# Kernel tuning notes

Hardware: AMD Instinct MI355X
Metric: run time of the kernel (lower is better)

The kernel has to match this reference:

```python
import jax, jax.numpy as jnp
import numpy as np

B, T, I, H, O = 64, 2048, 128, 256, 128
K1 = 1
K2 = 1


def setup_inputs() -> dict:
    key = jax.random.key(0)
    ks = jax.random.split(key, 8)
    M = H - K1 + 1
    return {
        "x": jax.random.normal(ks[0], (B, T, I), jnp.float32),
        "W_in": jax.random.normal(ks[1], (H, I), jnp.float32) / np.sqrt(I).astype(np.float32),
        "b_in": jax.random.normal(ks[2], (H,), jnp.float32) * 0.01,
        "W_out": jax.random.normal(ks[3], (O, H), jnp.float32) / np.sqrt(H).astype(np.float32),
        "b_out": jax.random.normal(ks[4], (O,), jnp.float32) * 0.01,
        # padded Householder vectors: row i uses its first K+i entries (masked in reference)
        # uniform in [0.5, 1.5] keeps u.u well away from 0 (avoids 2/<u,u> blowup)
        "u_raw": jax.random.uniform(ks[5], (M, H), jnp.float32, 0.5, 1.5),
        "sigmas": jnp.ones((H,), jnp.float32),
        "v_raw": jax.random.uniform(ks[6], (M, H), jnp.float32, 0.5, 1.5),
    }


def _householder_chain(hats):
    # U <- H_last @ ... @ H_0, H_i = I - 2/<u,u> u u^T, applied as rank-1 updates
    Hdim = hats.shape[1]
    def step(Umat, u):
        beta = 2.0 / jnp.dot(u, u)
        return Umat - beta * jnp.outer(u, u @ Umat), None
    U, _ = jax.lax.scan(step, jnp.eye(Hdim, dtype=hats.dtype), hats)
    return U


def reference(x, W_in, b_in, W_out, b_out, u_raw, sigmas, v_raw):
    Hdim = sigmas.shape[0]
    Mu = u_raw.shape[0]
    Mv = v_raw.shape[0]
    # row i of u_hats has entries in cols [0, K1+i), then flipped along cols
    mask_u = jnp.arange(Hdim)[None, :] < (K1 + jnp.arange(Mu))[:, None]
    u_hats = jnp.flip(jnp.where(mask_u, u_raw, 0.0), axis=1)
    mask_v = jnp.arange(Hdim)[None, :] < (K2 + jnp.arange(Mv))[:, None]
    v_hats = jnp.flip(jnp.where(mask_v, v_raw, 0.0), axis=(0, 1))  # torch.flip dims=[0,1]
    U = _householder_chain(u_hats)
    V = _householder_chain(v_hats)
    W = (U * sigmas[None, :]) @ V  # U @ diag(sigmas) @ V
    # precompute input projection for all timesteps: [T, B, H]
    xproj = jnp.einsum('bti,hi->tbh', x, W_in) + b_in
    h0 = jnp.zeros((x.shape[0], Hdim), x.dtype)
    def cell(h, xp):
        h = jnp.tanh(xp + h @ W.T)
        return h, h @ W_out.T + b_out
    _, out = jax.lax.scan(cell, h0, xproj)  # out: [T, B, O]
    return jnp.transpose(out, (1, 0, 2))
```

## Files before the change

### kernel.cpp

```cpp
#include <hip/hip_runtime.h>
#include <hip/hip_bf16.h>
#include <hip/hip_fp16.h>

#define BB 64
#define TT 2048
#define II 128
#define HH 256
#define OO 128
#define RCH 8

typedef _Float16 f16x2 __attribute__((ext_vector_type(2)));

#if __has_builtin(__builtin_amdgcn_fdot2)
__device__ __forceinline__ float fdot2(f16x2 a, f16x2 b, float c) {
    return __builtin_amdgcn_fdot2(a, b, c, false);
}
#else
__device__ __forceinline__ float fdot2(f16x2 a, f16x2 b, float c) {
    return fmaf((float)a.x, (float)b.x, fmaf((float)a.y, (float)b.y, c));
}
#endif

__device__ __forceinline__ f16x2 u2h(unsigned int u) { return __builtin_bit_cast(f16x2, u); }
__device__ __forceinline__ unsigned int packf16(float a, float b) {
    return __builtin_bit_cast(unsigned int, f16x2{(_Float16)a, (_Float16)b});
}

__device__ __forceinline__ float tanh_fast(float x) {
    float xc = fminf(fmaxf(x, -9.0f), 9.0f);
    float e = __expf(2.0f * xc);
    return (e - 1.0f) * __fdividef(1.0f, e + 1.0f);
}

__global__ __launch_bounds__(64) void prep_kernel(
    const float* __restrict__ u_raw, const float* __restrict__ v_raw,
    float* __restrict__ u_eff, float* __restrict__ v_eff,
    float* __restrict__ beta_u, float* __restrict__ beta_v)
{
    const int row = blockIdx.x;
    const int lane = threadIdx.x;
    const bool isU = row < HH;
    const int i = isU ? row : row - HH;
    const float* src = isU ? (u_raw + (size_t)i * HH) : (v_raw + (size_t)(HH - 1 - i) * HH);
    float* dst = (isU ? u_eff : v_eff) + (size_t)i * HH;
    const int lo = isU ? (HH - 1 - i) : i;
    float ss = 0.0f;
    for (int c = lane; c < HH; c += 64) {
        float vv = (c >= lo) ? src[HH - 1 - c] : 0.0f;
        dst[c] = vv;
        ss += vv * vv;
    }
    for (int m = 1; m < 64; m <<= 1) ss += __shfl_xor(ss, m, 64);
    if (lane == 0) (isU ? beta_u : beta_v)[i] = 2.0f / ss;
}

__global__ __launch_bounds__(256) void hh_kernel(
    const float* __restrict__ u_eff, const float* __restrict__ v_eff,
    const float* __restrict__ beta_u, const float* __restrict__ beta_v,
    float* __restrict__ Ucol, float* __restrict__ Vrow)
{
    const int wid = blockIdx.x * 4 + (threadIdx.x >> 6);
    const int lane = threadIdx.x & 63;
    const bool isU = wid < HH;
    const int j = isU ? wid : wid - HH;
    const float* eff = isU ? u_eff : v_eff;
    const float* beta = isU ? beta_u : beta_v;

    float cr0 = (j == 4 * lane + 0) ? 1.0f : 0.0f;
    float cr1 = (j == 4 * lane + 1) ? 1.0f : 0.0f;
    float cr2 = (j == 4 * lane + 2) ? 1.0f : 0.0f;
    float cr3 = (j == 4 * lane + 3) ? 1.0f : 0.0f;

    const int i0 = isU ? (HH - 1 - j) : 0;
    for (int i = i0; i < HH; ++i) {
        const float4 v4 = *(const float4*)(eff + (size_t)i * HH + lane * 4);
        float d = v4.x * cr0 + v4.y * cr1 + v4.z * cr2 + v4.w * cr3;
        for (int m = 1; m < 64; m <<= 1) d += __shfl_xor(d, m, 64);
        const float t = beta[i] * d;
        cr0 = fmaf(-t, v4.x, cr0);
        cr1 = fmaf(-t, v4.y, cr1);
        cr2 = fmaf(-t, v4.z, cr2);
        cr3 = fmaf(-t, v4.w, cr3);
    }
    if (isU) {
        *(float4*)(Ucol + (size_t)j * HH + lane * 4) = make_float4(cr0, cr1, cr2, cr3);
    } else {
        Vrow[(size_t)(4 * lane + 0) * HH + j] = cr0;
        Vrow[(size_t)(4 * lane + 1) * HH + j] = cr1;
        Vrow[(size_t)(4 * lane + 2) * HH + j] = cr2;
        Vrow[(size_t)(4 * lane + 3) * HH + j] = cr3;
    }
}

__global__ __launch_bounds__(256) void w_kernel(
    const float* __restrict__ Ucol, const float* __restrict__ Vrow,
    const float* __restrict__ sig, float* __restrict__ Wm)
{
    const int r = blockIdx.x;
    const int c = threadIdx.x;
    float acc = 0.0f;
    #pragma unroll 4
    for (int k = 0; k < HH; ++k) {
        acc = fmaf(Ucol[(size_t)k * HH + r] * sig[k], Vrow[(size_t)k * HH + c], acc);
    }
    Wm[(size_t)r * HH + c] = acc;
}

__device__ __forceinline__ uint4 stage8(const float* p) {
    float4 a = *(const float4*)p;
    float4 b = *(const float4*)(p + 4);
    return make_uint4(packf16(a.x, a.y), packf16(a.z, a.w),
                      packf16(b.x, b.y), packf16(b.z, b.w));
}
__device__ __forceinline__ uint4 stage8(const __half* p) {
    return *(const uint4*)p;
}
__device__ __forceinline__ void storeC(float* p, float v) { *p = v; }
__device__ __forceinline__ void storeC(__half* p, float v) { *p = __float2half_rn(v); }

template <typename AT, typename OT>
__global__ __launch_bounds__(256) void gemm_bias(
    const AT* __restrict__ A, const float* __restrict__ Bm,
    const float* __restrict__ bias, OT* __restrict__ C,
    int M, int N, int K)
{
    __shared__ unsigned int As[64][20];
    __shared__ unsigned int Bs[64][20];
    const int m0 = blockIdx.x * 64;
    const int n0 = blockIdx.y * 64;
    const int tid = threadIdx.x;
    const int lr = tid >> 2;
    const int lc = (tid & 3) << 3;
    const int tm = tid >> 4;
    const int tn = tid & 15;
    float acc[4][4] = {};
    for (int k0 = 0; k0 < K; k0 += 32) {
        *(uint4*)&As[lr][lc >> 1] = stage8(A + (size_t)(m0 + lr) * K + k0 + lc);
        *(uint4*)&Bs[lr][lc >> 1] = stage8(Bm + (size_t)(n0 + lr) * K + k0 + lc);
        __syncthreads();
        #pragma unroll
        for (int k8 = 0; k8 < 4; ++k8) {
            uint4 a4[4], b4[4];
            #pragma unroll
            for (int r = 0; r < 4; ++r) {
                a4[r] = *(const uint4*)&As[tm * 4 + r][k8 * 4];
                b4[r] = *(const uint4*)&Bs[tn + 16 * r][k8 * 4];
            }
            #pragma unroll
            for (int i2 = 0; i2 < 4; ++i2) {
                #pragma unroll
                for (int j2 = 0; j2 < 4; ++j2) {
                    acc[i2][j2] = fdot2(u2h(a4[i2].x), u2h(b4[j2].x), acc[i2][j2]);
                    acc[i2][j2] = fdot2(u2h(a4[i2].y), u2h(b4[j2].y), acc[i2][j2]);
                    acc[i2][j2] = fdot2(u2h(a4[i2].z), u2h(b4[j2].z), acc[i2][j2]);
                    acc[i2][j2] = fdot2(u2h(a4[i2].w), u2h(b4[j2].w), acc[i2][j2]);
                }
            }
        }
        __syncthreads();
    }
    #pragma unroll
    for (int j2 = 0; j2 < 4; ++j2) {
        const int n = n0 + tn + 16 * j2;
        const float bv = bias[n];
        #pragma unroll
        for (int i2 = 0; i2 < 4; ++i2) {
            const int m = m0 + tm * 4 + i2;
            storeC(C + (size_t)m * N + n, acc[i2][j2] + bv);
        }
    }
}

__global__ __launch_bounds__(512) void recur_kernel(
    const float* __restrict__ Wm,
    const __half* __restrict__ xp,
    __half* __restrict__ hall)
{
    const int b = blockIdx.x;
    const int tid = threadIdx.x;
    const int l = tid & 63;
    const int q = tid >> 6;
    const int lr = l & 31;
    const int half = l >> 5;
    const int row = 32 * q + lr;

    __shared__ float ps[2][8][HH];

    f16x2 w2[4][16];
    #pragma unroll
    for (int r = 0; r < 4; ++r) {
        const float* Wp = Wm + (size_t)(4 * l + r) * HH + q * 32;
        #pragma unroll
        for (int c4 = 0; c4 < 8; ++c4) {
            float4 f = *(const float4*)(Wp + c4 * 4);
            w2[r][c4 * 2 + 0] = f16x2{(_Float16)f.x, (_Float16)f.y};
            w2[r][c4 * 2 + 1] = f16x2{(_Float16)f.z, (_Float16)f.w};
        }
    }

    const unsigned short* xpw16 = (const unsigned short*)(xp + (size_t)b * TT * HH);
    unsigned short* hw16 = (unsigned short*)(hall + (size_t)b * TT * HH);

    unsigned short xpcur[RCH], xpnxt[RCH], hst[RCH];
    if (half == 0) {
        #pragma unroll
        for (int s = 0; s < RCH; ++s) xpcur[s] = xpw16[(size_t)s * HH + row];
    }

    f16x2 hv[16];
    #pragma unroll
    for (int i = 0; i < 16; ++i) hv[i] = f16x2{(_Float16)0.f, (_Float16)0.f};

    const int nch = TT / RCH;
    for (int c = 0; c < nch; ++c) {
        #pragma unroll
        for (int s = 0; s < RCH; ++s) {
            const int p = s & 1;
            if (s == 0 && half == 0 && c + 1 < nch) {
                const unsigned short* xn = xpw16 + (size_t)(c + 1) * RCH * HH + row;
                #pragma unroll
                for (int s2 = 0; s2 < RCH; ++s2) xpnxt[s2] = xn[(size_t)s2 * HH];
            }
            float a0 = 0.f, a1 = 0.f, a2 = 0.f, a3 = 0.f;
            #pragma unroll
            for (int cc = 0; cc < 16; ++cc) {
                a0 = fdot2(w2[0][cc], hv[cc], a0);
                a1 = fdot2(w2[1][cc], hv[cc], a1);
                a2 = fdot2(w2[2][cc], hv[cc], a2);
                a3 = fdot2(w2[3][cc], hv[cc], a3);
            }
            *(float4*)(&ps[p][q][4 * l]) = make_float4(a0, a1, a2, a3);
            __syncthreads();

            const float* pb = &ps[p][4 * half][row];
            float r0 = pb[0 * HH], r1 = pb[1 * HH], r2 = pb[2 * HH], r3 = pb[3 * HH];
            float s4 = (r0 + r1) + (r2 + r3);
            float tot = s4 + __shfl_xor(s4, 32, 64);
            float xv = 0.f;
            if (half == 0) {
                __half_raw hr; hr.x = xpcur[s];
                xv = (float)(*(const _Float16*)&hr.x);
            }
            float hn = tanh_fast(tot + xv);
            if (half == 0) {
                f16x2 t2{(_Float16)hn, (_Float16)0.f};
                hst[s] = (unsigned short)(__builtin_bit_cast(unsigned int, t2) & 0xffffu);
            }
            float hn1 = __shfl_down(hn, 1, 64);
            unsigned int packed = packf16(hn, hn1);
            #pragma unroll
            for (int i = 0; i < 16; ++i) {
                hv[i] = u2h((unsigned int)__builtin_amdgcn_readlane(packed, 2 * i));
            }
        }
        if (half == 0) {
            unsigned short* hwc = hw16 + (size_t)c * RCH * HH + row;
            #pragma unroll
            for (int s = 0; s < RCH; ++s) hwc[(size_t)s * HH] = hst[s];
            #pragma unroll
            for (int s = 0; s < RCH; ++s) xpcur[s] = xpnxt[s];
        }
    }
}

extern "C" void kernel_launch(void* const* d_in, const int* in_sizes, int n_in,
                              void* d_out, int out_size, void* d_ws, size_t ws_size,
                              hipStream_t stream) {
    const float* x     = (const float*)d_in[0];
    const float* W_in  = (const float*)d_in[1];
    const float* b_in  = (const float*)d_in[2];
    const float* W_out = (const float*)d_in[3];
    const float* b_out = (const float*)d_in[4];
    const float* u_raw = (const float*)d_in[5];
    const float* sig   = (const float*)d_in[6];
    const float* v_raw = (const float*)d_in[7];
    float* out = (float*)d_out;

    char* ws = (char*)d_ws;
    size_t off = 0;
    auto alloc = [&](size_t bytes) -> void* {
        void* p = (void*)(ws + off);
        off += (bytes + 255) & ~((size_t)255);
        return p;
    };
    float* u_eff  = (float*)alloc((size_t)HH * HH * 4);
    float* v_eff  = (float*)alloc((size_t)HH * HH * 4);
    float* beta_u = (float*)alloc((size_t)HH * 4);
    float* beta_v = (float*)alloc((size_t)HH * 4);
    float* Ucol   = (float*)alloc((size_t)HH * HH * 4);
    float* Vrow   = (float*)alloc((size_t)HH * HH * 4);
    float* Wm     = (float*)alloc((size_t)HH * HH * 4);
    __half* xpbuf = (__half*)alloc((size_t)BB * TT * HH * 2);
    __half* hall  = (__half*)alloc((size_t)BB * TT * HH * 2);
    (void)ws_size; (void)in_sizes; (void)n_in; (void)out_size;

    prep_kernel<<<2 * HH, 64, 0, stream>>>(u_raw, v_raw, u_eff, v_eff, beta_u, beta_v);
    hh_kernel<<<(2 * HH) / 4, 256, 0, stream>>>(u_eff, v_eff, beta_u, beta_v, Ucol, Vrow);
    w_kernel<<<HH, HH, 0, stream>>>(Ucol, Vrow, sig, Wm);
    gemm_bias<float, __half>
        <<<dim3((BB * TT) / 64, HH / 64), 256, 0, stream>>>(x, W_in, b_in, xpbuf, BB * TT, HH, II);
    recur_kernel<<<BB, 512, 0, stream>>>(Wm, xpbuf, hall);
    gemm_bias<__half, float>
        <<<dim3((BB * TT) / 64, OO / 64), 256, 0, stream>>>(hall, W_out, b_out, out, BB * TT, OO, HH);
}
```

Baseline: 1.595 ms.

## Batch 16 sequences per block and run the recurrence matvec with MFMA

Replaces the per-sequence fdot2 recurrence kernel, which used one block per batch element, with a kernel that groups 16 batch elements per block. Each step's h@W^T is computed as 16x16x32 f16 MFMA tiles, with W fragments held in registers and h staged through a 9-deep ring buffer in LDS. Hidden states are written out in coalesced 16-byte chunks once per 8-step chunk, and the ring buffer replaces the partial-sum reduction and readlane broadcast. The grid shrinks from 64 blocks to 4, so far fewer CUs are busy, and each step still needs a block-wide barrier.

```diff
diff --git a/kernel.cpp b/kernel.cpp
--- a/kernel.cpp
+++ b/kernel.cpp
@@ -7,9 +7,15 @@
 #define II 128
 #define HH 256
 #define OO 128
+
+#define BGRP 16
 #define RCH 8
+#define NBUF 9
+#define HPAD 264
 
 typedef _Float16 f16x2 __attribute__((ext_vector_type(2)));
+typedef _Float16 f16x8 __attribute__((ext_vector_type(8)));
+typedef float f32x4 __attribute__((ext_vector_type(4)));
 
 #if __has_builtin(__builtin_amdgcn_fdot2)
 __device__ __forceinline__ float fdot2(f16x2 a, f16x2 b, float c) {
@@ -171,94 +177,99 @@
     }
 }
 
-__global__ __launch_bounds__(512) void recur_kernel(
+__global__ __launch_bounds__(512, 2) void recur_mfma(
     const float* __restrict__ Wm,
     const __half* __restrict__ xp,
     __half* __restrict__ hall)
 {
-    const int b = blockIdx.x;
+    const int bg = blockIdx.x;
     const int tid = threadIdx.x;
-    const int l = tid & 63;
-    const int q = tid >> 6;
-    const int lr = l & 31;
-    const int half = l >> 5;
-    const int row = 32 * q + lr;
-
-    __shared__ float ps[2][8][HH];
-
-    f16x2 w2[4][16];
+    const int lane = tid & 63;
+    const int w = tid >> 6;
+    const int lo = lane & 15;
+    const int qd = lane >> 4;
+
+    __shared__ _Float16 hlds[NBUF][BGRP][HPAD];
+
+    f16x8 wf[2][8];
     #pragma unroll
-    for (int r = 0; r < 4; ++r) {
-        const float* Wp = Wm + (size_t)(4 * l + r) * HH + q * 32;
-        #pragma unroll
-        for (int c4 = 0; c4 < 8; ++c4) {
-            float4 f = *(const float4*)(Wp + c4 * 4);
-            w2[r][c4 * 2 + 0] = f16x2{(_Float16)f.x, (_Float16)f.y};
-            w2[r][c4 * 2 + 1] = f16x2{(_Float16)f.z, (_Float16)f.w};
-        }
-    }
-
-    const unsigned short* xpw16 = (const unsigned short*)(xp + (size_t)b * TT * HH);
-    unsigned short* hw16 = (unsigned short*)(hall + (size_t)b * TT * HH);
-
-    unsigned short xpcur[RCH], xpnxt[RCH], hst[RCH];
-    if (half == 0) {
-        #pragma unroll
-        for (int s = 0; s < RCH; ++s) xpcur[s] = xpw16[(size_t)s * HH + row];
-    }
-
-    f16x2 hv[16];
+    for (int tt = 0; tt < 2; ++tt) {
+        const float* wp = Wm + (size_t)(16 * (2 * w + tt) + lo) * HH + qd * 8;
+        #pragma unroll
+        for (int kb = 0; kb < 8; ++kb) {
+            float4 f0 = *(const float4*)(wp + kb * 32);
+            float4 f1 = *(const float4*)(wp + kb * 32 + 4);
+            wf[tt][kb] = f16x8{(_Float16)f0.x, (_Float16)f0.y, (_Float16)f0.z, (_Float16)f0.w,
+                               (_Float16)f1.x, (_Float16)f1.y, (_Float16)f1.z, (_Float16)f1.w};
+        }
+    }
+    for (int i = tid; i < BGRP * HPAD / 2; i += 512)
+        ((unsigned int*)&hlds[NBUF - 1][0][0])[i] = 0u;
+
+    const int b_abs = BGRP * bg + lo;
+    const __half* xb = xp + (size_t)b_abs * TT * HH;
+    const int j0 = 32 * w + 4 * qd;
+
+    uint2 xpc[2][RCH], xpn[2][RCH];
     #pragma unroll
-    for (int i = 0; i < 16; ++i) hv[i] = f16x2{(_Float16)0.f, (_Float16)0.f};
+    for (int s = 0; s < RCH; ++s) {
+        xpc[0][s] = *(const uint2*)(xb + (size_t)s * HH + j0);
+        xpc[1][s] = *(const uint2*)(xb + (size_t)s * HH + j0 + 16);
+    }
+    __syncthreads();
 
     const int nch = TT / RCH;
     for (int c = 0; c < nch; ++c) {
         #pragma unroll
         for (int s = 0; s < RCH; ++s) {
-            const int p = s & 1;
-            if (s == 0 && half == 0 && c + 1 < nch) {
-                const unsigned short* xn = xpw16 + (size_t)(c + 1) * RCH * HH + row;
+            const int gs = c * RCH + s;
+            const int rb = (gs + NBUF - 1) % NBUF;
+            const int wb = gs % NBUF;
+            if (s == 0 && c + 1 < nch) {
+                const __half* xn = xb + (size_t)(c + 1) * RCH * HH;
                 #pragma unroll
-                for (int s2 = 0; s2 < RCH; ++s2) xpnxt[s2] = xn[(size_t)s2 * HH];
-            }
-            float a0 = 0.f, a1 = 0.f, a2 = 0.f, a3 = 0.f;
-            #pragma unroll
-            for (int cc = 0; cc < 16; ++cc) {
-                a0 = fdot2(w2[0][cc], hv[cc], a0);
-                a1 = fdot2(w2[1][cc], hv[cc], a1);
-                a2 = fdot2(w2[2][cc], hv[cc], a2);
-                a3 = fdot2(w2[3][cc], hv[cc], a3);
-            }
-            *(float4*)(&ps[p][q][4 * l]) = make_float4(a0, a1, a2, a3);
+                for (int s2 = 0; s2 < RCH; ++s2) {
+                    xpn[0][s2] = *(const uint2*)(xn + (size_t)s2 * HH + j0);
+                    xpn[1][s2] = *(const uint2*)(xn + (size_t)s2 * HH + j0 + 16);
+                }
+            }
+            f16x8 hb[8];
+            const _Float16* hr = &hlds[rb][lo][qd * 8];
+            #pragma unroll
+            for (int kb = 0; kb < 8; ++kb)
+                hb[kb] = *(const f16x8*)(hr + kb * 32);
+            uint2 xa = xpc[0][s], xbv = xpc[1][s];
+            f32x4 acc0 = {(float)u2h(xa.x).x, (float)u2h(xa.x).y,
+                          (float)u2h(xa.y).x, (float)u2h(xa.y).y};
+            f32x4 acc1 = {(float)u2h(xbv.x).x, (float)u2h(xbv.x).y,
+                          (float)u2h(xbv.y).x, (float)u2h(xbv.y).y};
+            #pragma unroll
+            for (int kb = 0; kb < 8; ++kb) {
+                acc0 = __builtin_amdgcn_mfma_f32_16x16x32_f16(wf[0][kb], hb[kb], acc0, 0, 0, 0);
+                acc1 = __builtin_amdgcn_mfma_f32_16x16x32_f16(wf[1][kb], hb[kb], acc1, 0, 0, 0);
+            }
+            unsigned int p00 = packf16(tanh_fast(acc0.x), tanh_fast(acc0.y));
+            unsigned int p01 = packf16(tanh_fast(acc0.z), tanh_fast(acc0.w));
+            unsigned int p10 = packf16(tanh_fast(acc1.x), tanh_fast(acc1.y));
+            unsigned int p11 = packf16(tanh_fast(acc1.z), tanh_fast(acc1.w));
+            *(uint2*)&hlds[wb][lo][j0]      = make_uint2(p00, p01);
+            *(uint2*)&hlds[wb][lo][j0 + 16] = make_uint2(p10, p11);
             __syncthreads();
-
-            const float* pb = &ps[p][4 * half][row];
-            float r0 = pb[0 * HH], r1 = pb[1 * HH], r2 = pb[2 * HH], r3 = pb[3 * HH];
-            float s4 = (r0 + r1) + (r2 + r3);
-            float tot = s4 + __shfl_xor(s4, 32, 64);
-            float xv = 0.f;
-            if (half == 0) {
-                __half_raw hr; hr.x = xpcur[s];
-                xv = (float)(*(const _Float16*)&hr.x);
-            }
-            float hn = tanh_fast(tot + xv);
-            if (half == 0) {
-                f16x2 t2{(_Float16)hn, (_Float16)0.f};
-                hst[s] = (unsigned short)(__builtin_bit_cast(unsigned int, t2) & 0xffffu);
-            }
-            float hn1 = __shfl_down(hn, 1, 64);
-            unsigned int packed = packf16(hn, hn1);
-            #pragma unroll
-            for (int i = 0; i < 16; ++i) {
-                hv[i] = u2h((unsigned int)__builtin_amdgcn_readlane(packed, 2 * i));
-            }
-        }
-        if (half == 0) {
-            unsigned short* hwc = hw16 + (size_t)c * RCH * HH + row;
-            #pragma unroll
-            for (int s = 0; s < RCH; ++s) hwc[(size_t)s * HH] = hst[s];
-            #pragma unroll
-            for (int s = 0; s < RCH; ++s) xpcur[s] = xpnxt[s];
+        }
+        {
+            const int bb = tid >> 5;
+            const int jseg = tid & 31;
+            #pragma unroll
+            for (int s2 = 0; s2 < RCH; ++s2) {
+                const int gs2 = c * RCH + s2;
+                uint4 v = *(const uint4*)&hlds[gs2 % NBUF][bb][jseg * 8];
+                *(uint4*)(hall + ((size_t)(BGRP * bg + bb) * TT + gs2) * HH + jseg * 8) = v;
+            }
+        }
+        #pragma unroll
+        for (int s2 = 0; s2 < RCH; ++s2) {
+            xpc[0][s2] = xpn[0][s2];
+            xpc[1][s2] = xpn[1][s2];
         }
     }
 }
@@ -299,7 +310,7 @@
     w_kernel<<<HH, HH, 0, stream>>>(Ucol, Vrow, sig, Wm);
     gemm_bias<float, __half>
         <<<dim3((BB * TT) / 64, HH / 64), 256, 0, stream>>>(x, W_in, b_in, xpbuf, BB * TT, HH, II);
-    recur_kernel<<<BB, 512, 0, stream>>>(Wm, xpbuf, hall);
+    recur_mfma<<<BB / BGRP, 512, 0, stream>>>(Wm, xpbuf, hall);
     gemm_bias<__half, float>
         <<<dim3((BB * TT) / 64, OO / 64), 256, 0, stream>>>(hall, W_out, b_out, out, BB * TT, OO, HH);
 }
```

After: 3.079 ms. +93.1%, slower.
